# Optimization experiments

Measured on AMD Instinct MI355X. Metric: run time of the kernel, lower is better.

## Reference

```python
import jax, jax.numpy as jnp
import numpy as np

HEAD = 128
E = 1536
MAXPOS = 2048

def _rope_tables(seq_len, d):
    # get_sinusoid_encoding_table: col 2i = sin(pos/10000^(2i/d)), col 2i+1 = cos(same)
    pos = np.arange(seq_len, dtype=np.float32)[:, None]
    i = np.arange(d // 2, dtype=np.float32)
    ang = pos / np.power(10000.0, 2.0 * i / d)  # [seq, d/2]
    cos_pos = np.repeat(np.cos(ang), 2, axis=-1)  # table[:,1::2] repeat_interleave(2)
    sin_pos = np.repeat(np.sin(ang), 2, axis=-1)  # table[:,0::2] repeat_interleave(2)
    return jnp.asarray(cos_pos), jnp.asarray(sin_pos)

def _apply_rope(x, cos_pos, sin_pos):
    # x: [b, s, d]; rotate pairs (x0,x1) -> (-x1, x0)
    x2 = jnp.stack([-x[..., 1::2], x[..., ::2]], axis=-1).reshape(x.shape)
    return x * cos_pos + x2 * sin_pos

def setup_inputs() -> dict:
    key = jax.random.key(0)
    ks = jax.random.split(key, 6)
    b, s, h = 4, 2048, 768
    return {
        "hidden_states": jax.random.normal(ks[0], (b, s, h), jnp.float32),
        "attention_mask": jnp.ones((b, 1, 1, s), jnp.float32),
        "Wi": jax.random.normal(ks[1], (h, 2 * E + HEAD), jnp.float32) * 0.02,
        "bi": jnp.zeros((2 * E + HEAD,), jnp.float32),
        "gamma": 1.0 + jax.random.normal(ks[2], (2, HEAD), jnp.float32) * 0.02,
        "beta": jnp.zeros((2, HEAD), jnp.float32),
        "Wo": jax.random.normal(ks[3], (E, h), jnp.float32) * 0.02,
        "bo": jnp.zeros((h,), jnp.float32),
    }

def reference(hidden_states, attention_mask, Wi, bi, gamma, beta, Wo, bo):
    b, s, _ = hidden_states.shape
    x = jax.nn.silu(hidden_states @ Wi + bi)  # hidden_act='swish'
    u, v, qk = jnp.split(x, [E, 2 * E], axis=-1)  # [b,s,E],[b,s,E],[b,s,HEAD]
    # OffsetScale with 2 heads -> q, k
    q = qk * gamma[0] + beta[0]
    k = qk * gamma[1] + beta[1]
    cos_pos, sin_pos = _rope_tables(s, HEAD)
    q = _apply_rope(q, cos_pos, sin_pos)
    k = _apply_rope(k, cos_pos, sin_pos)
    scores = jnp.einsum('bid,bjd->bij', q, k) / jnp.sqrt(jnp.float32(HEAD))
    add_mask = (1.0 - attention_mask) * -1e12  # [b,1,1,s]
    scores = scores + jnp.squeeze(add_mask, axis=1)  # broadcast [b,1,s]
    # softmax_plus normalization
    valid = (scores > -1e11).astype(scores.dtype)
    l = jnp.maximum(jnp.sum(valid, axis=-1, keepdims=True), 1.0)
    scale = jnp.log(l) / jnp.log(jnp.float32(512.0))
    attn = jax.nn.softmax(scores * scale, axis=-1)
    out = (u * jnp.einsum('bij,bjd->bid', attn, v)) @ Wo + bo
    return out
```

## Files before the change

kernel.cpp:

```cpp
#include <hip/hip_runtime.h>
#include <math.h>

typedef _Float16 f16;
typedef _Float16 f16x8 __attribute__((ext_vector_type(8)));
typedef float f32x4 __attribute__((ext_vector_type(4)));

#define HEAD 128
#define EDIM 1536
#define NI   3200
#define HDIM 768
#define BATCH 4
#define SEQ  2048
#define MTOT (BATCH*SEQ)

__device__ __forceinline__ void gld_lds16(const void* g, void* l) {
  __builtin_amdgcn_global_load_lds(
      (const __attribute__((address_space(1))) void*)g,
      (__attribute__((address_space(3))) void*)l, 16, 0, 0);
}

__global__ __launch_bounds__(256) void cast_f32_f16_k(const float* __restrict__ in,
                                                      f16* __restrict__ out, int n4) {
  int i = blockIdx.x * 256 + threadIdx.x;
  if (i >= n4) return;
  float4 x = ((const float4*)in)[i];
  union { f16 h[4]; short4 s; } u;
  u.h[0] = (f16)x.x; u.h[1] = (f16)x.y; u.h[2] = (f16)x.z; u.h[3] = (f16)x.w;
  ((short4*)out)[i] = u.s;
}

__global__ __launch_bounds__(256) void transpose_cast_k(const float* __restrict__ in, int ld_in,
                                                        f16* __restrict__ out, int ld_out) {
  __shared__ float tile[32][33];
  int c = threadIdx.x & 31, r0 = threadIdx.x >> 5;
  int ib = blockIdx.y * 32, jb = blockIdx.x * 32;
#pragma unroll
  for (int rr = 0; rr < 32; rr += 8)
    tile[r0 + rr][c] = in[(size_t)(ib + r0 + rr) * ld_in + jb + c];
  __syncthreads();
#pragma unroll
  for (int rr = 0; rr < 32; rr += 8)
    out[(size_t)(jb + r0 + rr) * ld_out + ib + c] = (f16)tile[c][r0 + rr];
}

__global__ __launch_bounds__(256) void transpose_f16_k(const f16* __restrict__ in, int ld_in,
                                                       long long sIn,
                                                       f16* __restrict__ out, int ld_out,
                                                       long long sOut) {
  __shared__ f16 tile[32][33];
  in  += (size_t)blockIdx.z * sIn;
  out += (size_t)blockIdx.z * sOut;
  int c = threadIdx.x & 31, r0 = threadIdx.x >> 5;
  int ib = blockIdx.y * 32, jb = blockIdx.x * 32;
#pragma unroll
  for (int rr = 0; rr < 32; rr += 8)
    tile[r0 + rr][c] = in[(size_t)(ib + r0 + rr) * ld_in + jb + c];
  __syncthreads();
#pragma unroll
  for (int rr = 0; rr < 32; rr += 8)
    out[(size_t)(jb + r0 + rr) * ld_out + ib + c] = tile[c][r0 + rr];
}

__global__ __launch_bounds__(256) void rope_tables_k(float* __restrict__ cosT,
                                                     float* __restrict__ sinT) {
  int id = blockIdx.x * 256 + threadIdx.x;
  int pos = id >> 6, i = id & 63;
  float ang = (float)pos / powf(10000.0f, (float)(2 * i) / 128.0f);
  float cv = cosf(ang), sv = sinf(ang);
  cosT[pos * HEAD + 2 * i]     = cv;
  cosT[pos * HEAD + 2 * i + 1] = cv;
  sinT[pos * HEAD + 2 * i]     = sv;
  sinT[pos * HEAD + 2 * i + 1] = sv;
}

__global__ __launch_bounds__(256) void addmask_k(const float* __restrict__ mask,
                                                 float* __restrict__ am) {
  int i = blockIdx.x * 256 + threadIdx.x;
  am[i] = (1.0f - mask[i]) * -1e12f;
}

template <int MODE>
__global__ __launch_bounds__(256, 4)
void gemm_bt(const f16* __restrict__ A, int lda,
             const f16* __restrict__ Bt, int ldb, int K,
             float* __restrict__ outF,
             f16* __restrict__ outH, f16* __restrict__ outH2, f16* __restrict__ outH3,
             const float* __restrict__ c0, const float* __restrict__ c1,
             const float* __restrict__ c2, const float* __restrict__ c3,
             const float* __restrict__ c4) {
  __shared__ f16 As0[128 * 32], As1[128 * 32], Bs0[128 * 32], Bs1[128 * 32];
  int bx, by;
  {
    int gx = gridDim.x;
    int id = blockIdx.y * gx + blockIdx.x;
    int cpx = (gx * gridDim.y) >> 3;
    int sw = (id & 7) * cpx + (id >> 3);
    bx = sw % gx; by = sw / gx;
  }
  const int m0 = by * 128, n0 = bx * 128;
  const int t = threadIdx.x;
  const int lane = t & 63, w = t >> 6;
  const int wr = w >> 1, wc = w & 1;
  const int lr = lane & 15, kg = lane >> 4;

  const f16* ga = A  + (size_t)(m0 + (t >> 2)) * lda + (t & 3) * 8;
  const f16* gb = Bt + (size_t)(n0 + (t >> 2)) * ldb + (t & 3) * 8;

  f32x4 acc[4][4];
#pragma unroll
  for (int i = 0; i < 4; ++i)
#pragma unroll
    for (int j = 0; j < 4; ++j) acc[i][j] = f32x4{0.f, 0.f, 0.f, 0.f};

  auto stage = [&](f16* AS, f16* BS, int kk) {
    gld_lds16(ga + kk,                    (char*)AS + w * 1024);
    gld_lds16(ga + (size_t)64 * lda + kk, (char*)AS + w * 1024 + 4096);
    gld_lds16(gb + kk,                    (char*)BS + w * 1024);
    gld_lds16(gb + (size_t)64 * ldb + kk, (char*)BS + w * 1024 + 4096);
  };
  auto compute = [&](const f16* AS, const f16* BS) {
    f16x8 af[4], bf[4];
#pragma unroll
    for (int i = 0; i < 4; ++i) {
      af[i] = *(const f16x8*)&AS[(wr * 64 + i * 16 + lr) * 32 + kg * 8];
      bf[i] = *(const f16x8*)&BS[(wc * 64 + i * 16 + lr) * 32 + kg * 8];
    }
#pragma unroll
    for (int i = 0; i < 4; ++i)
#pragma unroll
      for (int j = 0; j < 4; ++j)
        acc[i][j] = __builtin_amdgcn_mfma_f32_16x16x32_f16(af[i], bf[j], acc[i][j], 0, 0, 0);
  };

  stage(As0, Bs0, 0);
  __syncthreads();
  for (int k0 = 0; k0 < K; k0 += 64) {
    if (k0 + 32 < K) stage(As1, Bs1, k0 + 32);
    compute(As0, Bs0);
    __syncthreads();
    if (k0 + 64 < K) stage(As0, Bs0, k0 + 64);
    compute(As1, Bs1);
    __syncthreads();
  }

#pragma unroll
  for (int i = 0; i < 4; ++i) {
#pragma unroll
    for (int j = 0; j < 4; ++j) {
#pragma unroll
      for (int r = 0; r < 4; ++r) {
        int row = m0 + wr * 64 + i * 16 + kg * 4 + r;
        int col = n0 + wc * 64 + j * 16 + lr;
        float x = acc[i][j][r];
        if (MODE == 0) {
          float xb = x + c0[col];
          float s = xb * __builtin_amdgcn_rcpf(1.0f + __expf(-xb));
          if (bx == 24) {
            int c = col - 3072;
            float pv = __shfl_xor(s, 1, 64);
            int pos = row & (SEQ - 1);
            float cv = c3[pos * HEAD + c], sv = c4[pos * HEAD + c];
            float q  = s  * c1[c]       + c2[c];
            float pq = pv * c1[c ^ 1]   + c2[c ^ 1];
            float x2q = (c & 1) ? pq : -pq;
            outH2[row * HEAD + c] = (f16)(q * cv + x2q * sv);
            float kk = s  * c1[128 + c]       + c2[128 + c];
            float pk = pv * c1[128 + (c ^ 1)] + c2[128 + (c ^ 1)];
            float x2k = (c & 1) ? pk : -pk;
            outH3[row * HEAD + c] = (f16)(kk * cv + x2k * sv);
          } else {
            outH[(size_t)row * 3072 + col] = (f16)s;
          }
        } else {
          outF[(size_t)row * HDIM + col] = x + c0[col];
        }
      }
    }
  }
}

__global__ __launch_bounds__(256, 4)
void gemm_scores(const f16* __restrict__ Q, const f16* __restrict__ Kt,
                 f16* __restrict__ P, const float* __restrict__ am) {
  __shared__ f16 As0[128 * 32], As1[128 * 32], Bs0[128 * 32], Bs1[128 * 32];
  const int z = blockIdx.z;
  int bx, by;
  {
    int gx = gridDim.x;
    int id = blockIdx.y * gx + blockIdx.x;
    int cpx = (gx * gridDim.y) >> 3;
    int sw = (id & 7) * cpx + (id >> 3);
    bx = sw % gx; by = sw / gx;
  }
  const int m0 = by * 128, n0 = bx * 128;
  const int t = threadIdx.x;
  const int lane = t & 63, w = t >> 6;
  const int wr = w >> 1, wc = w & 1;
  const int lr = lane & 15, kg = lane >> 4;

  const f16* A = Q  + (size_t)z * SEQ * HEAD;
  const f16* B = Kt + (size_t)z * SEQ * HEAD;
  const f16* ga = A + (size_t)(m0 + (t >> 2)) * HEAD + (t & 3) * 8;
  const f16* gb = B + (size_t)(n0 + (t >> 2)) * HEAD + (t & 3) * 8;

  f32x4 acc[4][4];
#pragma unroll
  for (int i = 0; i < 4; ++i)
#pragma unroll
    for (int j = 0; j < 4; ++j) acc[i][j] = f32x4{0.f, 0.f, 0.f, 0.f};

  auto stage = [&](f16* AS, f16* BS, int kk) {
    gld_lds16(ga + kk,                     (char*)AS + w * 1024);
    gld_lds16(ga + (size_t)64 * HEAD + kk, (char*)AS + w * 1024 + 4096);
    gld_lds16(gb + kk,                     (char*)BS + w * 1024);
    gld_lds16(gb + (size_t)64 * HEAD + kk, (char*)BS + w * 1024 + 4096);
  };
  auto compute = [&](const f16* AS, const f16* BS) {
    f16x8 af[4], bf[4];
#pragma unroll
    for (int i = 0; i < 4; ++i) {
      af[i] = *(const f16x8*)&AS[(wr * 64 + i * 16 + lr) * 32 + kg * 8];
      bf[i] = *(const f16x8*)&BS[(wc * 64 + i * 16 + lr) * 32 + kg * 8];
    }
#pragma unroll
    for (int i = 0; i < 4; ++i)
#pragma unroll
      for (int j = 0; j < 4; ++j)
        acc[i][j] = __builtin_amdgcn_mfma_f32_16x16x32_f16(af[i], bf[j], acc[i][j], 0, 0, 0);
  };

  stage(As0, Bs0, 0);
  __syncthreads();
  for (int k0 = 0; k0 < HEAD; k0 += 64) {
    if (k0 + 32 < HEAD) stage(As1, Bs1, k0 + 32);
    compute(As0, Bs0);
    __syncthreads();
    if (k0 + 64 < HEAD) stage(As0, Bs0, k0 + 64);
    compute(As1, Bs1);
    __syncthreads();
  }

  f16* outP = P + (size_t)z * SEQ * SEQ;
  const float* c = am + (size_t)z * SEQ;
#pragma unroll
  for (int i = 0; i < 4; ++i)
#pragma unroll
    for (int j = 0; j < 4; ++j)
#pragma unroll
      for (int r = 0; r < 4; ++r) {
        int row = m0 + wr * 64 + i * 16 + kg * 4 + r;
        int col = n0 + wc * 64 + j * 16 + lr;
        outP[(size_t)row * SEQ + col] = (f16)(acc[i][j][r] * 0.08838834764831845f + c[col]);
      }
}

template <int MODE>
__global__ __launch_bounds__(512, 2)
void gemm8p(const f16* __restrict__ A, int lda,
            const f16* __restrict__ B0, int ldb, long long sB, int bshift, int K,
            f16* __restrict__ outH, const f16* __restrict__ hA) {
  __shared__ f16 LS[2][2][2][2][4096];
  int bx, by;
  {
    int gx = gridDim.x;
    int id = blockIdx.y * gx + blockIdx.x;
    int cpx = (gx * gridDim.y) >> 3;
    int sw = (id & 7) * cpx + (id >> 3);
    bx = sw % gx; by = sw / gx;
  }
  const int m0 = by * 256, n0 = bx * 256;
  const int t = threadIdx.x;
  const int lane = t & 63, w = t >> 6;
  const int wr = w >> 2, wc = w & 3;
  const int lr = lane & 15, kg = lane >> 4;
  const int bb = by >> bshift;
  const f16* Bb = B0 + (size_t)bb * sB;

  const int rb = t >> 3;
  const int sl = ((t & 7) ^ (rb & 7)) << 3;
  const f16* gA = A  + (size_t)(m0 + rb) * lda + sl;
  const f16* gB = Bb + (size_t)(n0 + rb) * ldb + sl;
  char* lA = (char*)LS + w * 1024;
  char* lB = (char*)LS + 32768 + w * 1024;

  auto stageA = [&](int kt, int h) {
    const f16* s = gA + (size_t)(h << 7) * lda + (kt << 6);
    char* d = lA + ((kt & 1) << 16) + (h << 14);
    gld_lds16(s, d);
    gld_lds16(s + ((size_t)lda << 6), d + 8192);
  };
  auto stageB = [&](int kt, int h) {
    const f16* s = gB + (size_t)(h << 7) * ldb + (kt << 6);
    char* d = lB + ((kt & 1) << 16) + (h << 14);
    gld_lds16(s, d);
    gld_lds16(s + ((size_t)ldb << 6), d + 8192);
  };

  const char* RA = (const char*)LS + ((wr * 128 + lr) << 7);
  const char* RB = (const char*)LS + 32768 + ((wc * 64 + lr) << 7);
  const int sw0 = (kg ^ (lr & 7)) << 4;
  const int sw1 = ((4 + kg) ^ (lr & 7)) << 4;

  f32x4 acc[8][4];
#pragma unroll
  for (int i = 0; i < 8; ++i)
#pragma unroll
    for (int j = 0; j < 4; ++j) acc[i][j] = f32x4{0.f, 0.f, 0.f, 0.f};

  const int nt = K >> 6;
  stageA(0, 0); stageA(0, 1); stageB(0, 0); stageB(0, 1);
  asm volatile("" ::: "memory");
  if (nt > 1) {
    stageB(1, 0); stageB(1, 1);
    asm volatile("s_waitcnt vmcnt(4)" ::: "memory");
  } else {
    asm volatile("s_waitcnt vmcnt(0)" ::: "memory");
  }
  __builtin_amdgcn_s_barrier();
  asm volatile("" ::: "memory");

  for (int tt = 0; tt < nt; ++tt) {
    const char* SA = RA + ((tt & 1) << 16);
    const char* SB = RB + ((tt & 1) << 16);
    f16x8 a0[4][2], a1[4][2], b0[2][2], b1[2][2];
#pragma unroll
    for (int i2 = 0; i2 < 4; ++i2) {
      a0[i2][0] = *(const f16x8*)(SA + (i2 << 11) + sw0);
      a0[i2][1] = *(const f16x8*)(SA + (i2 << 11) + sw1);
    }
#pragma unroll
    for (int j2 = 0; j2 < 2; ++j2) {
      b0[j2][0] = *(const f16x8*)(SB + (j2 << 11) + sw0);
      b0[j2][1] = *(const f16x8*)(SB + (j2 << 11) + sw1);
    }
    if (tt + 1 < nt) stageA(tt + 1, 0);
    __builtin_amdgcn_s_barrier();
    asm volatile("" ::: "memory");
    __builtin_amdgcn_s_setprio(1);
#pragma unroll
    for (int ks = 0; ks < 2; ++ks)
#pragma unroll
      for (int i2 = 0; i2 < 4; ++i2)
#pragma unroll
        for (int j2 = 0; j2 < 2; ++j2)
          acc[i2][j2] = __builtin_amdgcn_mfma_f32_16x16x32_f16(
              a0[i2][ks], b0[j2][ks], acc[i2][j2], 0, 0, 0);
    __builtin_amdgcn_s_setprio(0);
    __builtin_amdgcn_s_barrier();
    asm volatile("" ::: "memory");
#pragma unroll
    for (int j2 = 0; j2 < 2; ++j2) {
      b1[j2][0] = *(const f16x8*)(SB + ((2 + j2) << 11) + sw0);
      b1[j2][1] = *(const f16x8*)(SB + ((2 + j2) << 11) + sw1);
    }
    if (tt + 1 < nt) stageA(tt + 1, 1);
    __builtin_amdgcn_s_barrier();
    asm volatile("" ::: "memory");
    __builtin_amdgcn_s_setprio(1);
#pragma unroll
    for (int ks = 0; ks < 2; ++ks)
#pragma unroll
      for (int i2 = 0; i2 < 4; ++i2)
#pragma unroll
        for (int j2 = 0; j2 < 2; ++j2)
          acc[i2][2 + j2] = __builtin_amdgcn_mfma_f32_16x16x32_f16(
              a0[i2][ks], b1[j2][ks], acc[i2][2 + j2], 0, 0, 0);
    __builtin_amdgcn_s_setprio(0);
    __builtin_amdgcn_s_barrier();
    asm volatile("" ::: "memory");
#pragma unroll
    for (int i2 = 0; i2 < 4; ++i2) {
      a1[i2][0] = *(const f16x8*)(SA + ((4 + i2) << 11) + sw0);
      a1[i2][1] = *(const f16x8*)(SA + ((4 + i2) << 11) + sw1);
    }
    if (tt + 2 < nt) stageB(tt + 2, 0);
    __builtin_amdgcn_s_barrier();
    asm volatile("" ::: "memory");
    __builtin_amdgcn_s_setprio(1);
#pragma unroll
    for (int ks = 0; ks < 2; ++ks)
#pragma unroll
      for (int i2 = 0; i2 < 4; ++i2)
#pragma unroll
        for (int j2 = 0; j2 < 2; ++j2)
          acc[4 + i2][j2] = __builtin_amdgcn_mfma_f32_16x16x32_f16(
              a1[i2][ks], b0[j2][ks], acc[4 + i2][j2], 0, 0, 0);
    __builtin_amdgcn_s_setprio(0);
    __builtin_amdgcn_s_barrier();
    asm volatile("" ::: "memory");
    if (tt + 2 < nt) stageB(tt + 2, 1);
    __builtin_amdgcn_s_barrier();
    asm volatile("" ::: "memory");
    __builtin_amdgcn_s_setprio(1);
#pragma unroll
    for (int ks = 0; ks < 2; ++ks)
#pragma unroll
      for (int i2 = 0; i2 < 4; ++i2)
#pragma unroll
        for (int j2 = 0; j2 < 2; ++j2)
          acc[4 + i2][2 + j2] = __builtin_amdgcn_mfma_f32_16x16x32_f16(
              a1[i2][ks], b1[j2][ks], acc[4 + i2][2 + j2], 0, 0, 0);
    __builtin_amdgcn_s_setprio(0);
    if (tt + 2 < nt) asm volatile("s_waitcnt vmcnt(4)" ::: "memory");
    else             asm volatile("s_waitcnt vmcnt(0)" ::: "memory");
    __builtin_amdgcn_s_barrier();
    asm volatile("" ::: "memory");
  }

  const int colbase = n0 + wc * 64;
#pragma unroll
  for (int i = 0; i < 8; ++i) {
#pragma unroll
    for (int j = 0; j < 4; ++j) {
#pragma unroll
      for (int r = 0; r < 4; ++r) {
        int row = m0 + wr * 128 + i * 16 + kg * 4 + r;
        int col = colbase + j * 16 + lr;
        float uu = (float)hA[(size_t)row * 3072 + col];
        outH[(size_t)row * EDIM + col] = (f16)(acc[i][j][r] * uu);
      }
    }
  }
}

__global__ __launch_bounds__(256) void softmax_plus_f16(f16* __restrict__ P) {
  __shared__ float red[4];
  const int t = threadIdx.x;
  f16* pr = P + (size_t)blockIdx.x * SEQ;
  union { uint4 u4; f16 h[8]; } ld;
  ld.u4 = ((const uint4*)pr)[t];
  float v[8];
#pragma unroll
  for (int i = 0; i < 8; ++i) v[i] = fmaxf((float)ld.h[i], -1e12f);

  float cnt = 0.f;
#pragma unroll
  for (int i = 0; i < 8; ++i) cnt += (v[i] > -1e11f) ? 1.0f : 0.0f;
#pragma unroll
  for (int o = 32; o; o >>= 1) cnt += __shfl_xor(cnt, o, 64);
  if ((t & 63) == 0) red[t >> 6] = cnt;
  __syncthreads();
  cnt = red[0] + red[1] + red[2] + red[3];
  float scale = __logf(fmaxf(cnt, 1.0f)) * 0.16025848f;

  float mx = -INFINITY;
#pragma unroll
  for (int i = 0; i < 8; ++i) { v[i] *= scale; mx = fmaxf(mx, v[i]); }
#pragma unroll
  for (int o = 32; o; o >>= 1) mx = fmaxf(mx, __shfl_xor(mx, o, 64));
  __syncthreads();
  if ((t & 63) == 0) red[t >> 6] = mx;
  __syncthreads();
  mx = fmaxf(fmaxf(red[0], red[1]), fmaxf(red[2], red[3]));

  float p[8], sum = 0.f;
#pragma unroll
  for (int i = 0; i < 8; ++i) { p[i] = __expf(v[i] - mx); sum += p[i]; }
#pragma unroll
  for (int o = 32; o; o >>= 1) sum += __shfl_xor(sum, o, 64);
  __syncthreads();
  if ((t & 63) == 0) red[t >> 6] = sum;
  __syncthreads();
  sum = red[0] + red[1] + red[2] + red[3];
  float inv = __builtin_amdgcn_rcpf(sum);

  union { f16 h[8]; uint4 u4; } pk;
#pragma unroll
  for (int i = 0; i < 8; ++i) pk.h[i] = (f16)(p[i] * inv);
  ((uint4*)pr)[t] = pk.u4;
}

extern "C" void kernel_launch(void* const* d_in, const int* in_sizes, int n_in,
                              void* d_out, int out_size, void* d_ws, size_t ws_size,
                              hipStream_t stream) {
  const float* hs    = (const float*)d_in[0];
  const float* mask  = (const float*)d_in[1];
  const float* Wi    = (const float*)d_in[2];
  const float* bi    = (const float*)d_in[3];
  const float* gamma = (const float*)d_in[4];
  const float* beta  = (const float*)d_in[5];
  const float* Wo    = (const float*)d_in[6];
  const float* bo    = (const float*)d_in[7];
  float* out = (float*)d_out;

  const int nb = (ws_size >= ((size_t)170 << 20)) ? BATCH : 1;

  char* p = (char*)d_ws;
  auto alloc = [&](size_t b) { char* r = p; p += (b + 255) & ~(size_t)255; return r; };
  f16*   Xh   = (f16*)  alloc((size_t)MTOT * 3072 * 2);
  f16*   Qh   = (f16*)  alloc((size_t)MTOT * HEAD * 2);
  f16*   Kh   = (f16*)  alloc((size_t)MTOT * HEAD * 2);
  f16*   Ah   = (f16*)  alloc((size_t)MTOT * HDIM * 2);
  f16*   WiT  = (f16*)  alloc((size_t)NI * HDIM * 2);
  f16*   WoT  = (f16*)  alloc((size_t)HDIM * EDIM * 2);
  float* cosT = (float*)alloc((size_t)SEQ * HEAD * 4);
  float* sinT = (float*)alloc((size_t)SEQ * HEAD * 4);
  float* am   = (float*)alloc((size_t)BATCH * SEQ * 4);
  f16*   G    = (f16*)  alloc((size_t)MTOT * EDIM * 2);
  f16*   P    = (f16*)  alloc((size_t)nb * SEQ * SEQ * 2);
  f16*   Vt   = (f16*)  alloc((size_t)nb * EDIM * SEQ * 2);

  cast_f32_f16_k<<<dim3(MTOT * HDIM / 4 / 256), 256, 0, stream>>>(hs, Ah, MTOT * HDIM / 4);
  transpose_cast_k<<<dim3(NI / 32, HDIM / 32), 256, 0, stream>>>(Wi, NI, WiT, HDIM);
  transpose_cast_k<<<dim3(HDIM / 32, EDIM / 32), 256, 0, stream>>>(Wo, HDIM, WoT, EDIM);
  rope_tables_k<<<dim3(SEQ * 64 / 256), 256, 0, stream>>>(cosT, sinT);
  addmask_k<<<dim3(BATCH * SEQ / 256), 256, 0, stream>>>(mask, am);

  gemm_bt<0><<<dim3(NI / 128, MTOT / 128), 256, 0, stream>>>(
      Ah, HDIM, WiT, HDIM, HDIM,
      nullptr, Xh, Qh, Kh, bi, gamma, beta, cosT, sinT);

  const int bsh = (nb == BATCH) ? 3 : 30;
  for (int b0 = 0; b0 < BATCH; b0 += nb) {
    transpose_f16_k<<<dim3(EDIM / 32, SEQ / 32, nb), 256, 0, stream>>>(
        Xh + (size_t)b0 * SEQ * 3072 + 1536, 3072, (long long)SEQ * 3072,
        Vt, SEQ, (long long)EDIM * SEQ);
    gemm_scores<<<dim3(SEQ / 128, SEQ / 128, nb), 256, 0, stream>>>(
        Qh + (size_t)b0 * SEQ * HEAD, Kh + (size_t)b0 * SEQ * HEAD,
        P, am + b0 * SEQ);
    softmax_plus_f16<<<dim3(nb * SEQ), 256, 0, stream>>>(P);
    gemm8p<2><<<dim3(EDIM / 256, nb * SEQ / 256), 512, 0, stream>>>(
        P, SEQ, Vt, SEQ, (long long)EDIM * SEQ, bsh, SEQ,
        G + (size_t)b0 * SEQ * EDIM,
        Xh + (size_t)b0 * SEQ * 3072);
  }

  gemm_bt<3><<<dim3(HDIM / 128, MTOT / 128), 256, 0, stream>>>(
      G, EDIM, WoT, EDIM, EDIM,
      out, nullptr, nullptr, nullptr, bo, nullptr, nullptr, nullptr, nullptr);
}
```

Measured before the change: 251.4 us.

## Replace input GEMM with single-wave triple-buffered kernel and one-shot scores tile

The input projection GEMM becomes a one-wavefront 64x64-tile kernel with a three-stage LDS ring, pipelined by vmcnt waits instead of block barriers, and an XCD-aware tile mapping. The scores GEMM loads the whole 128x128 Q and K tiles into LDS at once with an XOR swizzle to avoid bank conflicts, then runs all four K steps with no further barriers. The final projection is split into its own non-templated kernel. Smaller tiles add more global reloads of A and B and a large grid, in exchange for fewer syncs and more latency hiding.

```diff
diff --git a/kernel.cpp b/kernel.cpp
--- a/kernel.cpp
+++ b/kernel.cpp
@@ -79,32 +79,120 @@
   am[i] = (1.0f - mask[i]) * -1e12f;
 }
 
-template <int MODE>
-__global__ __launch_bounds__(256, 4)
-void gemm_bt(const f16* __restrict__ A, int lda,
-             const f16* __restrict__ Bt, int ldb, int K,
-             float* __restrict__ outF,
-             f16* __restrict__ outH, f16* __restrict__ outH2, f16* __restrict__ outH3,
-             const float* __restrict__ c0, const float* __restrict__ c1,
-             const float* __restrict__ c2, const float* __restrict__ c3,
-             const float* __restrict__ c4) {
-  __shared__ f16 As0[128 * 32], As1[128 * 32], Bs0[128 * 32], Bs1[128 * 32];
-  int bx, by;
-  {
-    int gx = gridDim.x;
-    int id = blockIdx.y * gx + blockIdx.x;
-    int cpx = (gx * gridDim.y) >> 3;
-    int sw = (id & 7) * cpx + (id >> 3);
-    bx = sw % gx; by = sw / gx;
-  }
-  const int m0 = by * 128, n0 = bx * 128;
+__global__ __launch_bounds__(64, 2)
+void gemm1_w1(const f16* __restrict__ A, const f16* __restrict__ Bt,
+              f16* __restrict__ outH, f16* __restrict__ outH2, f16* __restrict__ outH3,
+              const float* __restrict__ c0, const float* __restrict__ c1,
+              const float* __restrict__ c2, const float* __restrict__ c3,
+              const float* __restrict__ c4) {
+  __shared__ f16 LA[3][64 * 32];
+  __shared__ f16 LB[3][64 * 32];
+  const int id = blockIdx.x;
+  const int xcd = id & 7;
+  const int idx = id >> 3;
+  const int m0 = (xcd * 16 + (idx & 15)) << 6;
+  const int n0 = (idx >> 4) << 6;
+  const int lane = threadIdx.x;
+  const int lr = lane & 15, kg = lane >> 4;
+
+  const f16* gA = A  + (size_t)(m0 + (lane >> 2)) * HDIM + (lane & 3) * 8;
+  const f16* gB = Bt + (size_t)(n0 + (lane >> 2)) * HDIM + (lane & 3) * 8;
+
+  f32x4 acc[4][4];
+#pragma unroll
+  for (int i = 0; i < 4; ++i)
+#pragma unroll
+    for (int j = 0; j < 4; ++j) acc[i][j] = f32x4{0.f, 0.f, 0.f, 0.f};
+
+  auto stage = [&](int t, int b) {
+    char* dA = (char*)LA[b];
+    char* dB = (char*)LB[b];
+#pragma unroll
+    for (int c = 0; c < 4; ++c) {
+      gld_lds16(gA + (size_t)(c * 16) * HDIM + t * 32, dA + c * 1024);
+      gld_lds16(gB + (size_t)(c * 16) * HDIM + t * 32, dB + c * 1024);
+    }
+  };
+
+  const int nt = HDIM / 32;
+  stage(0, 0); stage(1, 1);
+  int buf = 0, nbuf = 2;
+  for (int t = 0; t < nt; ++t) {
+    if (t + 1 < nt) asm volatile("s_waitcnt vmcnt(8)" ::: "memory");
+    else            asm volatile("s_waitcnt vmcnt(0)" ::: "memory");
+    const f16* SA = LA[buf];
+    const f16* SB = LB[buf];
+    f16x8 af[4], bf[4];
+#pragma unroll
+    for (int i = 0; i < 4; ++i) {
+      af[i] = *(const f16x8*)&SA[(i * 16 + lr) * 32 + kg * 8];
+      bf[i] = *(const f16x8*)&SB[(i * 16 + lr) * 32 + kg * 8];
+    }
+    if (t + 2 < nt) stage(t + 2, nbuf);
+#pragma unroll
+    for (int i = 0; i < 4; ++i)
+#pragma unroll
+      for (int j = 0; j < 4; ++j)
+        acc[i][j] = __builtin_amdgcn_mfma_f32_16x16x32_f16(af[i], bf[j], acc[i][j], 0, 0, 0);
+    buf = (buf + 1) % 3; nbuf = (nbuf + 1) % 3;
+  }
+
+#pragma unroll
+  for (int i = 0; i < 4; ++i) {
+#pragma unroll
+    for (int j = 0; j < 4; ++j) {
+#pragma unroll
+      for (int r = 0; r < 4; ++r) {
+        int row = m0 + i * 16 + kg * 4 + r;
+        int col = n0 + j * 16 + lr;
+        float xb = acc[i][j][r] + c0[col];
+        float s = xb * __builtin_amdgcn_rcpf(1.0f + __expf(-xb));
+        if (n0 >= 3072) {
+          int c = col - 3072;
+          float pv = __shfl_xor(s, 1, 64);
+          int pos = row & (SEQ - 1);
+          float cv = c3[pos * HEAD + c], sv = c4[pos * HEAD + c];
+          float q  = s  * c1[c]       + c2[c];
+          float pq = pv * c1[c ^ 1]   + c2[c ^ 1];
+          float x2q = (c & 1) ? pq : -pq;
+          outH2[row * HEAD + c] = (f16)(q * cv + x2q * sv);
+          float kk = s  * c1[128 + c]       + c2[128 + c];
+          float pk = pv * c1[128 + (c ^ 1)] + c2[128 + (c ^ 1)];
+          float x2k = (c & 1) ? pk : -pk;
+          outH3[row * HEAD + c] = (f16)(kk * cv + x2k * sv);
+        } else {
+          outH[(size_t)row * 3072 + col] = (f16)s;
+        }
+      }
+    }
+  }
+}
+
+__global__ __launch_bounds__(256, 2)
+void scores_os(const f16* __restrict__ Q, const f16* __restrict__ Kt,
+               f16* __restrict__ P, const float* __restrict__ am) {
+  __shared__ f16 Qs[128 * 128];
+  __shared__ f16 Ks[128 * 128];
+  const int z = blockIdx.z;
+  const int m0 = blockIdx.y * 128, n0 = blockIdx.x * 128;
   const int t = threadIdx.x;
   const int lane = t & 63, w = t >> 6;
   const int wr = w >> 1, wc = w & 1;
   const int lr = lane & 15, kg = lane >> 4;
 
-  const f16* ga = A  + (size_t)(m0 + (t >> 2)) * lda + (t & 3) * 8;
-  const f16* gb = Bt + (size_t)(n0 + (t >> 2)) * ldb + (t & 3) * 8;
+  const f16* Qb = Q  + (size_t)z * SEQ * HEAD;
+  const f16* Kb = Kt + (size_t)z * SEQ * HEAD;
+
+  const int rq = t >> 4, l = t & 15;
+#pragma unroll
+  for (int c = 0; c < 8; ++c) {
+    int row = c * 16 + rq;
+    int lq = l ^ (row & 15);
+    gld_lds16(Qb + (size_t)(m0 + row) * HEAD + lq * 8, (char*)Qs + c * 4096 + w * 1024);
+    gld_lds16(Kb + (size_t)(n0 + row) * HEAD + lq * 8, (char*)Ks + c * 4096 + w * 1024);
+  }
+  asm volatile("s_waitcnt vmcnt(0)" ::: "memory");
+  __syncthreads();
 
   f32x4 acc[4][4];
 #pragma unroll
@@ -112,132 +200,21 @@
 #pragma unroll
     for (int j = 0; j < 4; ++j) acc[i][j] = f32x4{0.f, 0.f, 0.f, 0.f};
 
-  auto stage = [&](f16* AS, f16* BS, int kk) {
-    gld_lds16(ga + kk,                    (char*)AS + w * 1024);
-    gld_lds16(ga + (size_t)64 * lda + kk, (char*)AS + w * 1024 + 4096);
-    gld_lds16(gb + kk,                    (char*)BS + w * 1024);
-    gld_lds16(gb + (size_t)64 * ldb + kk, (char*)BS + w * 1024 + 4096);
-  };
-  auto compute = [&](const f16* AS, const f16* BS) {
+#pragma unroll
+  for (int kk = 0; kk < 4; ++kk) {
     f16x8 af[4], bf[4];
 #pragma unroll
     for (int i = 0; i < 4; ++i) {
-      af[i] = *(const f16x8*)&AS[(wr * 64 + i * 16 + lr) * 32 + kg * 8];
-      bf[i] = *(const f16x8*)&BS[(wc * 64 + i * 16 + lr) * 32 + kg * 8];
+      int rA = wr * 64 + i * 16 + lr;
+      af[i] = *(const f16x8*)&Qs[rA * 128 + (((kk * 4 + kg) ^ (rA & 15)) << 3)];
+      int rB = wc * 64 + i * 16 + lr;
+      bf[i] = *(const f16x8*)&Ks[rB * 128 + (((kk * 4 + kg) ^ (rB & 15)) << 3)];
     }
 #pragma unroll
     for (int i = 0; i < 4; ++i)
 #pragma unroll
       for (int j = 0; j < 4; ++j)
         acc[i][j] = __builtin_amdgcn_mfma_f32_16x16x32_f16(af[i], bf[j], acc[i][j], 0, 0, 0);
-  };
-
-  stage(As0, Bs0, 0);
-  __syncthreads();
-  for (int k0 = 0; k0 < K; k0 += 64) {
-    if (k0 + 32 < K) stage(As1, Bs1, k0 + 32);
-    compute(As0, Bs0);
-    __syncthreads();
-    if (k0 + 64 < K) stage(As0, Bs0, k0 + 64);
-    compute(As1, Bs1);
-    __syncthreads();
-  }
-
-#pragma unroll
-  for (int i = 0; i < 4; ++i) {
-#pragma unroll
-    for (int j = 0; j < 4; ++j) {
-#pragma unroll
-      for (int r = 0; r < 4; ++r) {
-        int row = m0 + wr * 64 + i * 16 + kg * 4 + r;
-        int col = n0 + wc * 64 + j * 16 + lr;
-        float x = acc[i][j][r];
-        if (MODE == 0) {
-          float xb = x + c0[col];
-          float s = xb * __builtin_amdgcn_rcpf(1.0f + __expf(-xb));
-          if (bx == 24) {
-            int c = col - 3072;
-            float pv = __shfl_xor(s, 1, 64);
-            int pos = row & (SEQ - 1);
-            float cv = c3[pos * HEAD + c], sv = c4[pos * HEAD + c];
-            float q  = s  * c1[c]       + c2[c];
-            float pq = pv * c1[c ^ 1]   + c2[c ^ 1];
-            float x2q = (c & 1) ? pq : -pq;
-            outH2[row * HEAD + c] = (f16)(q * cv + x2q * sv);
-            float kk = s  * c1[128 + c]       + c2[128 + c];
-            float pk = pv * c1[128 + (c ^ 1)] + c2[128 + (c ^ 1)];
-            float x2k = (c & 1) ? pk : -pk;
-            outH3[row * HEAD + c] = (f16)(kk * cv + x2k * sv);
-          } else {
-            outH[(size_t)row * 3072 + col] = (f16)s;
-          }
-        } else {
-          outF[(size_t)row * HDIM + col] = x + c0[col];
-        }
-      }
-    }
-  }
-}
-
-__global__ __launch_bounds__(256, 4)
-void gemm_scores(const f16* __restrict__ Q, const f16* __restrict__ Kt,
-                 f16* __restrict__ P, const float* __restrict__ am) {
-  __shared__ f16 As0[128 * 32], As1[128 * 32], Bs0[128 * 32], Bs1[128 * 32];
-  const int z = blockIdx.z;
-  int bx, by;
-  {
-    int gx = gridDim.x;
-    int id = blockIdx.y * gx + blockIdx.x;
-    int cpx = (gx * gridDim.y) >> 3;
-    int sw = (id & 7) * cpx + (id >> 3);
-    bx = sw % gx; by = sw / gx;
-  }
-  const int m0 = by * 128, n0 = bx * 128;
-  const int t = threadIdx.x;
-  const int lane = t & 63, w = t >> 6;
-  const int wr = w >> 1, wc = w & 1;
-  const int lr = lane & 15, kg = lane >> 4;
-
-  const f16* A = Q  + (size_t)z * SEQ * HEAD;
-  const f16* B = Kt + (size_t)z * SEQ * HEAD;
-  const f16* ga = A + (size_t)(m0 + (t >> 2)) * HEAD + (t & 3) * 8;
-  const f16* gb = B + (size_t)(n0 + (t >> 2)) * HEAD + (t & 3) * 8;
-
-  f32x4 acc[4][4];
-#pragma unroll
-  for (int i = 0; i < 4; ++i)
-#pragma unroll
-    for (int j = 0; j < 4; ++j) acc[i][j] = f32x4{0.f, 0.f, 0.f, 0.f};
-
-  auto stage = [&](f16* AS, f16* BS, int kk) {
-    gld_lds16(ga + kk,                     (char*)AS + w * 1024);
-    gld_lds16(ga + (size_t)64 * HEAD + kk, (char*)AS + w * 1024 + 4096);
-    gld_lds16(gb + kk,                     (char*)BS + w * 1024);
-    gld_lds16(gb + (size_t)64 * HEAD + kk, (char*)BS + w * 1024 + 4096);
-  };
-  auto compute = [&](const f16* AS, const f16* BS) {
-    f16x8 af[4], bf[4];
-#pragma unroll
-    for (int i = 0; i < 4; ++i) {
-      af[i] = *(const f16x8*)&AS[(wr * 64 + i * 16 + lr) * 32 + kg * 8];
-      bf[i] = *(const f16x8*)&BS[(wc * 64 + i * 16 + lr) * 32 + kg * 8];
-    }
-#pragma unroll
-    for (int i = 0; i < 4; ++i)
-#pragma unroll
-      for (int j = 0; j < 4; ++j)
-        acc[i][j] = __builtin_amdgcn_mfma_f32_16x16x32_f16(af[i], bf[j], acc[i][j], 0, 0, 0);
-  };
-
-  stage(As0, Bs0, 0);
-  __syncthreads();
-  for (int k0 = 0; k0 < HEAD; k0 += 64) {
-    if (k0 + 32 < HEAD) stage(As1, Bs1, k0 + 32);
-    compute(As0, Bs0);
-    __syncthreads();
-    if (k0 + 64 < HEAD) stage(As0, Bs0, k0 + 64);
-    compute(As1, Bs1);
-    __syncthreads();
   }
 
   f16* outP = P + (size_t)z * SEQ * SEQ;
@@ -421,6 +398,77 @@
       }
     }
   }
+}
+
+__global__ __launch_bounds__(256, 4)
+void gemm_final(const f16* __restrict__ A, int lda,
+                const f16* __restrict__ Bt, int ldb, int K,
+                float* __restrict__ outF, const float* __restrict__ c0) {
+  __shared__ f16 As0[128 * 32], As1[128 * 32], Bs0[128 * 32], Bs1[128 * 32];
+  int bx, by;
+  {
+    int gx = gridDim.x;
+    int id = blockIdx.y * gx + blockIdx.x;
+    int cpx = (gx * gridDim.y) >> 3;
+    int sw = (id & 7) * cpx + (id >> 3);
+    bx = sw % gx; by = sw / gx;
+  }
+  const int m0 = by * 128, n0 = bx * 128;
+  const int t = threadIdx.x;
+  const int lane = t & 63, w = t >> 6;
+  const int wr = w >> 1, wc = w & 1;
+  const int lr = lane & 15, kg = lane >> 4;
+
+  const f16* ga = A  + (size_t)(m0 + (t >> 2)) * lda + (t & 3) * 8;
+  const f16* gb = Bt + (size_t)(n0 + (t >> 2)) * ldb + (t & 3) * 8;
+
+  f32x4 acc[4][4];
+#pragma unroll
+  for (int i = 0; i < 4; ++i)
+#pragma unroll
+    for (int j = 0; j < 4; ++j) acc[i][j] = f32x4{0.f, 0.f, 0.f, 0.f};
+
+  auto stage = [&](f16* AS, f16* BS, int kk) {
+    gld_lds16(ga + kk,                    (char*)AS + w * 1024);
+    gld_lds16(ga + (size_t)64 * lda + kk, (char*)AS + w * 1024 + 4096);
+    gld_lds16(gb + kk,                    (char*)BS + w * 1024);
+    gld_lds16(gb + (size_t)64 * ldb + kk, (char*)BS + w * 1024 + 4096);
+  };
+  auto compute = [&](const f16* AS, const f16* BS) {
+    f16x8 af[4], bf[4];
+#pragma unroll
+    for (int i = 0; i < 4; ++i) {
+      af[i] = *(const f16x8*)&AS[(wr * 64 + i * 16 + lr) * 32 + kg * 8];
+      bf[i] = *(const f16x8*)&BS[(wc * 64 + i * 16 + lr) * 32 + kg * 8];
+    }
+#pragma unroll
+    for (int i = 0; i < 4; ++i)
+#pragma unroll
+      for (int j = 0; j < 4; ++j)
+        acc[i][j] = __builtin_amdgcn_mfma_f32_16x16x32_f16(af[i], bf[j], acc[i][j], 0, 0, 0);
+  };
+
+  stage(As0, Bs0, 0);
+  __syncthreads();
+  for (int k0 = 0; k0 < K; k0 += 64) {
+    if (k0 + 32 < K) stage(As1, Bs1, k0 + 32);
+    compute(As0, Bs0);
+    __syncthreads();
+    if (k0 + 64 < K) stage(As0, Bs0, k0 + 64);
+    compute(As1, Bs1);
+    __syncthreads();
+  }
+
+#pragma unroll
+  for (int i = 0; i < 4; ++i)
+#pragma unroll
+    for (int j = 0; j < 4; ++j)
+#pragma unroll
+      for (int r = 0; r < 4; ++r) {
+        int row = m0 + wr * 64 + i * 16 + kg * 4 + r;
+        int col = n0 + wc * 64 + j * 16 + lr;
+        outF[(size_t)row * HDIM + col] = acc[i][j][r] + c0[col];
+      }
 }
 
 __global__ __launch_bounds__(256) void softmax_plus_f16(f16* __restrict__ P) {
@@ -506,16 +554,15 @@
   rope_tables_k<<<dim3(SEQ * 64 / 256), 256, 0, stream>>>(cosT, sinT);
   addmask_k<<<dim3(BATCH * SEQ / 256), 256, 0, stream>>>(mask, am);
 
-  gemm_bt<0><<<dim3(NI / 128, MTOT / 128), 256, 0, stream>>>(
-      Ah, HDIM, WiT, HDIM, HDIM,
-      nullptr, Xh, Qh, Kh, bi, gamma, beta, cosT, sinT);
+  gemm1_w1<<<dim3(6400), 64, 0, stream>>>(
+      Ah, WiT, Xh, Qh, Kh, bi, gamma, beta, cosT, sinT);
 
   const int bsh = (nb == BATCH) ? 3 : 30;
   for (int b0 = 0; b0 < BATCH; b0 += nb) {
     transpose_f16_k<<<dim3(EDIM / 32, SEQ / 32, nb), 256, 0, stream>>>(
         Xh + (size_t)b0 * SEQ * 3072 + 1536, 3072, (long long)SEQ * 3072,
         Vt, SEQ, (long long)EDIM * SEQ);
-    gemm_scores<<<dim3(SEQ / 128, SEQ / 128, nb), 256, 0, stream>>>(
+    scores_os<<<dim3(SEQ / 128, SEQ / 128, nb), 256, 0, stream>>>(
         Qh + (size_t)b0 * SEQ * HEAD, Kh + (size_t)b0 * SEQ * HEAD,
         P, am + b0 * SEQ);
     softmax_plus_f16<<<dim3(nb * SEQ), 256, 0, stream>>>(P);
@@ -525,7 +572,6 @@
         Xh + (size_t)b0 * SEQ * 3072);
   }
 
-  gemm_bt<3><<<dim3(HDIM / 128, MTOT / 128), 256, 0, stream>>>(
-      G, EDIM, WoT, EDIM, EDIM,
-      out, nullptr, nullptr, nullptr, bo, nullptr, nullptr, nullptr, nullptr);
-}
+  gemm_final<<<dim3(HDIM / 128, MTOT / 128), 256, 0, stream>>>(
+      G, EDIM, WoT, EDIM, EDIM, out, bo);
+}
```

After: 264.4 us. +5.2%, slower.
